# Optimization experiments

Hardware: AMD Instinct MI355X
Metric: run time of the kernel (lower is better)

Reference implementation:

```python
import jax, jax.numpy as jnp
import numpy as np


def setup_inputs() -> dict:
    key = jax.random.key(0)
    k1, k2, k3 = jax.random.split(key, 3)
    x = jax.random.normal(k1, (8, 256, 256, 256), dtype=jnp.float32)
    # Conv2d(2, 1, kernel_size=7): kaiming-uniform-like small init
    fan_in = 2 * 7 * 7
    bound = 1.0 / np.sqrt(fan_in)
    conv_w = jax.random.uniform(k2, (1, 2, 7, 7), dtype=jnp.float32, minval=-bound, maxval=bound)
    conv_b = jax.random.uniform(k3, (1,), dtype=jnp.float32, minval=-bound, maxval=bound)
    return {"x": x, "conv_w": conv_w, "conv_b": conv_b}


def reference(x, conv_w, conv_b):
    # channel-wise mean and max -> [B, 2, H, W]
    avg_out = jnp.mean(x, axis=1, keepdims=True)
    max_out = jnp.max(x, axis=1, keepdims=True)
    stacked = jnp.concatenate([avg_out, max_out], axis=1)
    # 7x7 conv, 2->1 channels, padding=3 (SAME)
    attn = jax.lax.conv_general_dilated(
        stacked, conv_w,
        window_strides=(1, 1), padding=((3, 3), (3, 3)),
        dimension_numbers=("NCHW", "OIHW", "NCHW"),
    ) + conv_b[None, :, None, None]
    return jax.nn.sigmoid(attn) * x
```

## Files before the change

### kernel.cpp

```cpp
#include <hip/hip_runtime.h>
#include <math.h>

#define BB 8
#define CC 256
#define HH 256
#define WW 256
#define HWC (HH * WW)
#define BHW (BB * HWC)
#define CHW (CC * HWC)

__global__ __launch_bounds__(256) void k_stats(const float* __restrict__ x,
                                               float* __restrict__ avgp,
                                               float* __restrict__ maxp) {
    int g = blockIdx.x * 256 + threadIdx.x;
    if (g >= BHW / 4) return;
    int e   = g << 2;
    int b   = e >> 16;
    int pix = e & (HWC - 1);

    const float4* x4 = (const float4*)x + (((size_t)b * CHW + pix) >> 2);
    const int cstride = HWC >> 2;

    float4 v = x4[0];
    float4 s = v;
    float4 m = v;
#pragma unroll 4
    for (int c = 1; c < CC; ++c) {
        float4 t = x4[(size_t)c * cstride];
        s.x += t.x; s.y += t.y; s.z += t.z; s.w += t.w;
        m.x = fmaxf(m.x, t.x); m.y = fmaxf(m.y, t.y);
        m.z = fmaxf(m.z, t.z); m.w = fmaxf(m.w, t.w);
    }
    const float inv = 1.0f / (float)CC;
    float4 a = { s.x * inv, s.y * inv, s.z * inv, s.w * inv };
    ((float4*)avgp)[g] = a;
    ((float4*)maxp)[g] = m;
}

__global__ __launch_bounds__(256) void k_conv(const float* __restrict__ avgp,
                                              const float* __restrict__ maxp,
                                              const float* __restrict__ cw,
                                              const float* __restrict__ cb,
                                              float* __restrict__ attnp) {
    int t = blockIdx.x * 256 + threadIdx.x;
    if (t >= BHW) return;
    int b   = t >> 16;
    int pix = t & (HWC - 1);
    int h   = pix >> 8;
    int w   = pix & (WW - 1);

    const float* ap = avgp + (size_t)b * HWC;
    const float* mp = maxp + (size_t)b * HWC;

    float sum = cb[0];
#pragma unroll
    for (int kh = 0; kh < 7; ++kh) {
        int hh = h + kh - 3;
        if ((unsigned)hh >= (unsigned)HH) continue;
#pragma unroll
        for (int kw = 0; kw < 7; ++kw) {
            int ww = w + kw - 3;
            if ((unsigned)ww >= (unsigned)WW) continue;
            int o = (hh << 8) + ww;
            float wa = cw[kh * 7 + kw];
            float wm = cw[49 + kh * 7 + kw];
            sum = fmaf(wa, ap[o], sum);
            sum = fmaf(wm, mp[o], sum);
        }
    }
    attnp[t] = 1.0f / (1.0f + __expf(-sum));
}

__global__ __launch_bounds__(256) void k_mul(const float* __restrict__ x,
                                             const float* __restrict__ attnp,
                                             float* __restrict__ out) {
    size_t g = (size_t)blockIdx.x * 256 + threadIdx.x;
    size_t e = g << 2;
    size_t b   = e >> 24;
    size_t pix = e & (size_t)(HWC - 1);

    float4 a = *((const float4*)attnp + (((b << 16) + pix) >> 2));
    float4 v = ((const float4*)x)[g];
    float4 o = { v.x * a.x, v.y * a.y, v.z * a.z, v.w * a.w };
    ((float4*)out)[g] = o;
}

extern "C" void kernel_launch(void* const* d_in, const int* in_sizes, int n_in,
                              void* d_out, int out_size, void* d_ws, size_t ws_size,
                              hipStream_t stream) {
    const float* x  = (const float*)d_in[0];
    const float* cw = (const float*)d_in[1];
    const float* cb = (const float*)d_in[2];
    float* out = (float*)d_out;

    float* avgp  = (float*)d_ws;
    float* maxp  = avgp + BHW;
    float* attnp = maxp + BHW;

    {
        int nthreads = BHW / 4;
        int nblocks  = (nthreads + 255) / 256;
        k_stats<<<nblocks, 256, 0, stream>>>(x, avgp, maxp);
    }
    {
        int nblocks = (BHW + 255) / 256;
        k_conv<<<nblocks, 256, 0, stream>>>(avgp, maxp, cw, cb, attnp);
    }
    {
        long long total = (long long)BB * CHW / 4;
        int nblocks = (int)((total + 255) / 256);
        k_mul<<<nblocks, 256, 0, stream>>>(x, attnp, out);
    }
}
```

Before: 299.9 us.

## Process batch in chunks for cache reuse, split channel reduction, nontemporal output stores

The launch is restructured to run stats, conv and multiply per group of two batch images, so each image's input is re-read by the multiply kernel while it may still reside in the last-level cache. The stats kernel splits the channel reduction across four thread groups with a shared-memory combine, adding parallelism. Output is written with nontemporal stores to avoid evicting the input from cache. The cost is more kernel launches, and the cache reuse depends on the cache capacity holding the chunk.

```diff
diff --git a/kernel.cpp b/kernel.cpp
--- a/kernel.cpp
+++ b/kernel.cpp
@@ -6,51 +6,75 @@
 #define HH 256
 #define WW 256
 #define HWC (HH * WW)
-#define BHW (BB * HWC)
-#define CHW (CC * HWC)
+#define G4  (HWC / 4)
+
+#define GB 2
+
+typedef float nf4 __attribute__((ext_vector_type(4)));
 
 __global__ __launch_bounds__(256) void k_stats(const float* __restrict__ x,
                                                float* __restrict__ avgp,
-                                               float* __restrict__ maxp) {
-    int g = blockIdx.x * 256 + threadIdx.x;
-    if (g >= BHW / 4) return;
-    int e   = g << 2;
-    int b   = e >> 16;
-    int pix = e & (HWC - 1);
+                                               float* __restrict__ maxp,
+                                               int bbase) {
+    __shared__ float4 ssum[4][64];
+    __shared__ float4 smax[4][64];
 
-    const float4* x4 = (const float4*)x + (((size_t)b * CHW + pix) >> 2);
-    const int cstride = HWC >> 2;
+    const int gi = threadIdx.x & 63;
+    const int sp = threadIdx.x >> 6;
+    const int G  = blockIdx.x * 64 + gi;
+    const int bl = G >> 14;
+    const int p4 = G & (G4 - 1);
+    const int b  = bbase + bl;
+
+    const float4* x4 = (const float4*)x + (((size_t)b * CC + sp * 64) << 14) + p4;
 
     float4 v = x4[0];
-    float4 s = v;
-    float4 m = v;
+    float4 s = v, m = v;
 #pragma unroll 4
-    for (int c = 1; c < CC; ++c) {
-        float4 t = x4[(size_t)c * cstride];
+    for (int c = 1; c < 64; ++c) {
+        float4 t = x4[(size_t)c << 14];
         s.x += t.x; s.y += t.y; s.z += t.z; s.w += t.w;
         m.x = fmaxf(m.x, t.x); m.y = fmaxf(m.y, t.y);
         m.z = fmaxf(m.z, t.z); m.w = fmaxf(m.w, t.w);
     }
-    const float inv = 1.0f / (float)CC;
-    float4 a = { s.x * inv, s.y * inv, s.z * inv, s.w * inv };
-    ((float4*)avgp)[g] = a;
-    ((float4*)maxp)[g] = m;
+    ssum[sp][gi] = s;
+    smax[sp][gi] = m;
+    __syncthreads();
+
+    if (threadIdx.x < 64) {
+        float4 s0 = ssum[0][threadIdx.x], s1 = ssum[1][threadIdx.x];
+        float4 s2 = ssum[2][threadIdx.x], s3 = ssum[3][threadIdx.x];
+        float4 m0 = smax[0][threadIdx.x], m1 = smax[1][threadIdx.x];
+        float4 m2 = smax[2][threadIdx.x], m3 = smax[3][threadIdx.x];
+        const float inv = 1.0f / (float)CC;
+        float4 a = { (s0.x + s1.x + s2.x + s3.x) * inv,
+                     (s0.y + s1.y + s2.y + s3.y) * inv,
+                     (s0.z + s1.z + s2.z + s3.z) * inv,
+                     (s0.w + s1.w + s2.w + s3.w) * inv };
+        float4 mm = { fmaxf(fmaxf(m0.x, m1.x), fmaxf(m2.x, m3.x)),
+                      fmaxf(fmaxf(m0.y, m1.y), fmaxf(m2.y, m3.y)),
+                      fmaxf(fmaxf(m0.z, m1.z), fmaxf(m2.z, m3.z)),
+                      fmaxf(fmaxf(m0.w, m1.w), fmaxf(m2.w, m3.w)) };
+        size_t o = ((size_t)b << 14) + p4 - gi + threadIdx.x;
+        ((float4*)avgp)[o] = a;
+        ((float4*)maxp)[o] = mm;
+    }
 }
 
 __global__ __launch_bounds__(256) void k_conv(const float* __restrict__ avgp,
                                               const float* __restrict__ maxp,
                                               const float* __restrict__ cw,
                                               const float* __restrict__ cb,
-                                              float* __restrict__ attnp) {
-    int t = blockIdx.x * 256 + threadIdx.x;
-    if (t >= BHW) return;
+                                              float* __restrict__ attnp,
+                                              int bbase) {
+    int t = blockIdx.x * 256 + threadIdx.x + (bbase << 16);
     int b   = t >> 16;
     int pix = t & (HWC - 1);
     int h   = pix >> 8;
     int w   = pix & (WW - 1);
 
-    const float* ap = avgp + (size_t)b * HWC;
-    const float* mp = maxp + (size_t)b * HWC;
+    const float* ap = avgp + ((size_t)b << 16);
+    const float* mp = maxp + ((size_t)b << 16);
 
     float sum = cb[0];
 #pragma unroll
@@ -62,10 +86,8 @@
             int ww = w + kw - 3;
             if ((unsigned)ww >= (unsigned)WW) continue;
             int o = (hh << 8) + ww;
-            float wa = cw[kh * 7 + kw];
-            float wm = cw[49 + kh * 7 + kw];
-            sum = fmaf(wa, ap[o], sum);
-            sum = fmaf(wm, mp[o], sum);
+            sum = fmaf(cw[kh * 7 + kw],      ap[o], sum);
+            sum = fmaf(cw[49 + kh * 7 + kw], mp[o], sum);
         }
     }
     attnp[t] = 1.0f / (1.0f + __expf(-sum));
@@ -73,16 +95,18 @@
 
 __global__ __launch_bounds__(256) void k_mul(const float* __restrict__ x,
                                              const float* __restrict__ attnp,
-                                             float* __restrict__ out) {
-    size_t g = (size_t)blockIdx.x * 256 + threadIdx.x;
+                                             float* __restrict__ out,
+                                             int bbase) {
+    size_t g = ((size_t)blockIdx.x * 256 + threadIdx.x)
+             + (((size_t)bbase << 24) >> 2);
     size_t e = g << 2;
     size_t b   = e >> 24;
     size_t pix = e & (size_t)(HWC - 1);
 
     float4 a = *((const float4*)attnp + (((b << 16) + pix) >> 2));
     float4 v = ((const float4*)x)[g];
-    float4 o = { v.x * a.x, v.y * a.y, v.z * a.z, v.w * a.w };
-    ((float4*)out)[g] = o;
+    nf4 o = { v.x * a.x, v.y * a.y, v.z * a.z, v.w * a.w };
+    __builtin_nontemporal_store(o, (nf4*)out + g);
 }
 
 extern "C" void kernel_launch(void* const* d_in, const int* in_sizes, int n_in,
@@ -94,21 +118,12 @@
     float* out = (float*)d_out;
 
     float* avgp  = (float*)d_ws;
-    float* maxp  = avgp + BHW;
-    float* attnp = maxp + BHW;
+    float* maxp  = avgp + (size_t)BB * HWC;
+    float* attnp = maxp + (size_t)BB * HWC;
 
-    {
-        int nthreads = BHW / 4;
-        int nblocks  = (nthreads + 255) / 256;
-        k_stats<<<nblocks, 256, 0, stream>>>(x, avgp, maxp);
-    }
-    {
-        int nblocks = (BHW + 255) / 256;
-        k_conv<<<nblocks, 256, 0, stream>>>(avgp, maxp, cw, cb, attnp);
-    }
-    {
-        long long total = (long long)BB * CHW / 4;
-        int nblocks = (int)((total + 255) / 256);
-        k_mul<<<nblocks, 256, 0, stream>>>(x, attnp, out);
+    for (int bbase = 0; bbase < BB; bbase += GB) {
+        k_stats<<<GB * G4 / 64, 256, 0, stream>>>(x, avgp, maxp, bbase);
+        k_conv<<<GB * HWC / 256, 256, 0, stream>>>(avgp, maxp, cw, cb, attnp, bbase);
+        k_mul<<<GB * CC * (HWC / 4) / 256, 256, 0, stream>>>(x, attnp, out, bbase);
     }
 }
```

Result: slower. 311.8 us (+4.0%).
